# Optimization experiments

Measured on AMD Instinct MI355X. Metric: run time of the kernel, lower is better.

## Reference

```python
import jax, jax.numpy as jnp
import numpy as np


def setup_inputs() -> dict:
    key = jax.random.key(0)
    ks = jax.random.split(key, 6)
    B, U, E, D, P = 8, 1024, 1024, 256, 256
    return {
        "u_enc": jax.random.normal(ks[0], (B, U, D), dtype=jnp.float32),
        "e_enc": jax.random.normal(ks[1], (B, E, D), dtype=jnp.float32),
        "pair_enc": jax.random.normal(ks[2], (B, U, E), dtype=jnp.float32),
        "ue_mask": jax.random.uniform(ks[3], (B, U, E), dtype=jnp.float32),
        "w_kernel": jax.random.normal(ks[4], (D, P), dtype=jnp.float32) / np.sqrt(D).astype(np.float32),
        "w_bias": jnp.zeros((P,), dtype=jnp.float32),
        "bpp_w": jnp.ones((), dtype=jnp.float32),
        "bpp_b": jnp.zeros((), dtype=jnp.float32),
    }


def reference(u_enc, e_enc, pair_enc, ue_mask, w_kernel, w_bias, bpp_w, bpp_b):
    # OuterProductUpdate: shared Dense projection of u and e, then outer product.
    u_p = u_enc @ w_kernel + w_bias            # [B,U,P]
    e_p = e_enc @ w_kernel + w_bias            # [B,E,P]
    op = ue_mask * jnp.einsum('bup,bep->bue', u_p, e_p)  # [B,U,E]
    # Sigmoid gate over pair features.
    mask = ue_mask * jax.nn.sigmoid(bpp_w * pair_enc + bpp_b + op)  # [B,U,E]
    # Original: (mask[...,None] * concat(u_rep, e_rep)).sum(axis=(-2,-3)).
    # Algebraically identical without the UxEx2D intermediate:
    #   concat( sum_{u,e} mask * u_enc[u],  sum_{u,e} mask * e_enc[e] )
    u_part = jnp.einsum('bue,bud->bd', mask, u_enc)  # [B,D]
    e_part = jnp.einsum('bue,bed->bd', mask, e_enc)  # [B,D]
    return jnp.concatenate([u_part, e_part], axis=-1)  # [B,2D]
```

## Files before the change

### kernel.cpp

```cpp
#include <hip/hip_runtime.h>

#define BDIM 8
#define UDIM 1024
#define EDIM 1024
#define DDIM 256
#define PDIM 256

typedef __attribute__((ext_vector_type(8))) short bf16x8;
typedef __attribute__((ext_vector_type(4))) float f32x4;
typedef __attribute__((ext_vector_type(4))) unsigned short u16x4;

__device__ __forceinline__ short f2bf(float x) {
    unsigned u = __float_as_uint(x);
    unsigned r = (u + 0x7FFFu + ((u >> 16) & 1u)) >> 16;
    return (short)r;
}

__global__ __launch_bounds__(256) void prep_kernel(
    const float* __restrict__ w, ushort* __restrict__ wT,
    float* __restrict__ sums, float* __restrict__ out, int out_size)
{
    int n = blockIdx.x, k = threadIdx.x;
    wT[(size_t)n * PDIM + k] = (ushort)f2bf(w[(size_t)k * PDIM + n]);
    int g = n * 256 + k;
    if (g < BDIM * UDIM + BDIM * EDIM) sums[g] = 0.f;
    if (g < out_size) out[g] = 0.f;
}

__global__ __launch_bounds__(256) void proj_kernel(
    const float* __restrict__ u_enc, const float* __restrict__ e_enc,
    const ushort* __restrict__ wT, const float* __restrict__ bias,
    ushort* __restrict__ u_p, ushort* __restrict__ e_p)
{
    int row0 = blockIdx.x * 64;
    int col0 = blockIdx.y * 64;
    const float* A; ushort* C;
    if (row0 < BDIM * UDIM) { A = u_enc; C = u_p; }
    else                    { A = e_enc; C = e_p; row0 -= BDIM * UDIM; }

    int tid  = threadIdx.x;
    int wave = tid >> 6, lane = tid & 63;
    int m = lane & 15, quad = lane >> 4;

    const float*  aptr = A + (size_t)(row0 + wave * 16 + m) * DDIM + quad * 8;
    const ushort* bptr = wT + (size_t)(col0 + m * 4) * DDIM + quad * 8;

    float4 a[16];
    #pragma unroll
    for (int s = 0; s < 8; ++s) {
        a[2 * s]     = *(const float4*)(aptr + s * 32);
        a[2 * s + 1] = *(const float4*)(aptr + s * 32 + 4);
    }
    __builtin_amdgcn_sched_barrier(0);

    f32x4 acc[4] = {};

    #pragma unroll
    for (int s = 0; s < 8; ++s) {
        float4 a0 = a[2 * s], a1 = a[2 * s + 1];
        bf16x8 af;
        af[0] = f2bf(a0.x); af[1] = f2bf(a0.y); af[2] = f2bf(a0.z); af[3] = f2bf(a0.w);
        af[4] = f2bf(a1.x); af[5] = f2bf(a1.y); af[6] = f2bf(a1.z); af[7] = f2bf(a1.w);
        #pragma unroll
        for (int nt = 0; nt < 4; ++nt) {
            bf16x8 bfr = *(const bf16x8*)(bptr + (size_t)nt * DDIM + s * 32);
            acc[nt] = __builtin_amdgcn_mfma_f32_16x16x32_bf16(af, bfr, acc[nt], 0, 0, 0);
        }
    }

    float4 bv = *(const float4*)&bias[col0 + m * 4];
    #pragma unroll
    for (int r = 0; r < 4; ++r) {
        int row = row0 + wave * 16 + quad * 4 + r;
        u16x4 o;
        o[0] = (ushort)f2bf(acc[0][r] + bv.x);
        o[1] = (ushort)f2bf(acc[1][r] + bv.y);
        o[2] = (ushort)f2bf(acc[2][r] + bv.z);
        o[3] = (ushort)f2bf(acc[3][r] + bv.w);
        *(u16x4*)&C[(size_t)row * PDIM + col0 + m * 4] = o;
    }
}

__global__ __launch_bounds__(256) void fused_kernel(
    const ushort* __restrict__ u_p, const ushort* __restrict__ e_p,
    const float* __restrict__ pair_enc, const float* __restrict__ ue_mask,
    const float* __restrict__ bpp_w_p, const float* __restrict__ bpp_b_p,
    float* __restrict__ row_sums, float* __restrict__ col_sums)
{
    __shared__ float colred[4][64];

    int b  = blockIdx.y;
    int iu = blockIdx.x >> 4, ie = blockIdx.x & 15;
    int u0 = iu * 64, e0 = ie * 64;

    int tid  = threadIdx.x;
    int wave = tid >> 6, lane = tid & 63;
    int m = lane & 15, quad = lane >> 4;

    const float* pm = pair_enc + (size_t)b * UDIM * EDIM;
    const float* mm = ue_mask  + (size_t)b * UDIM * EDIM;

    float4 mv[4], pv[4];
    #pragma unroll
    for (int r = 0; r < 4; ++r) {
        size_t idx = (size_t)(u0 + wave * 16 + quad * 4 + r) * EDIM + e0 + m * 4;
        mv[r] = *(const float4*)&mm[idx];
        pv[r] = *(const float4*)&pm[idx];
    }
    __builtin_amdgcn_sched_barrier(0);

    const ushort* Au = u_p + (size_t)b * UDIM * PDIM + (size_t)(u0 + wave * 16 + m) * PDIM + quad * 8;
    const ushort* Be = e_p + (size_t)b * EDIM * PDIM + (size_t)(e0 + m * 4) * PDIM + quad * 8;

    f32x4 acc[4] = {};

    #pragma unroll
    for (int k0 = 0; k0 < PDIM; k0 += 32) {
        bf16x8 af = *(const bf16x8*)(Au + k0);
        #pragma unroll
        for (int nt = 0; nt < 4; ++nt) {
            bf16x8 bfr = *(const bf16x8*)(Be + (size_t)nt * PDIM + k0);
            acc[nt] = __builtin_amdgcn_mfma_f32_16x16x32_bf16(af, bfr, acc[nt], 0, 0, 0);
        }
    }

    float bw = bpp_w_p[0], bb = bpp_b_p[0];
    float rsum[4];
    float csum[4] = {0.f, 0.f, 0.f, 0.f};
    #pragma unroll
    for (int r = 0; r < 4; ++r) {
        float mvv[4] = {mv[r].x, mv[r].y, mv[r].z, mv[r].w};
        float pvv[4] = {pv[r].x, pv[r].y, pv[r].z, pv[r].w};
        float rs = 0.f;
        #pragma unroll
        for (int nt = 0; nt < 4; ++nt) {
            float arg = bw * pvv[nt] + bb + mvv[nt] * acc[nt][r];
            float s = mvv[nt] / (1.f + __expf(-arg));
            rs       += s;
            csum[nt] += s;
        }
        rsum[r] = rs;
    }

    #pragma unroll
    for (int r = 0; r < 4; ++r) {
        float v = rsum[r];
        v += __shfl_xor(v, 1); v += __shfl_xor(v, 2);
        v += __shfl_xor(v, 4); v += __shfl_xor(v, 8);
        if (m == 0)
            atomicAdd(&row_sums[(size_t)b * UDIM + u0 + wave * 16 + quad * 4 + r], v);
    }

    #pragma unroll
    for (int nt = 0; nt < 4; ++nt) {
        float v = csum[nt];
        v += __shfl_xor(v, 16); v += __shfl_xor(v, 32);
        if (quad == 0) colred[wave][m * 4 + nt] = v;
    }
    __syncthreads();

    if (tid < 64) {
        float v = colred[0][tid] + colred[1][tid] + colred[2][tid] + colred[3][tid];
        atomicAdd(&col_sums[(size_t)b * EDIM + e0 + tid], v);
    }
}

__global__ __launch_bounds__(256) void finish_kernel(
    const float* __restrict__ u_enc, const float* __restrict__ e_enc,
    const float* __restrict__ row_sums, const float* __restrict__ col_sums,
    float* __restrict__ out)
{
    int b = blockIdx.x;
    int half = blockIdx.y;
    int chunk = blockIdx.z;
    int d = threadIdx.x;

    const float* enc = half ? e_enc : u_enc;
    const float* s   = half ? col_sums : row_sums;

    int base = chunk * 16;
    float sv[16];
    #pragma unroll
    for (int u = 0; u < 16; ++u) sv[u] = s[(size_t)b * UDIM + base + u];

    float a0 = 0.f, a1 = 0.f, a2 = 0.f, a3 = 0.f;
    #pragma unroll
    for (int u = 0; u < 16; u += 4) {
        a0 += sv[u + 0] * enc[(size_t)(b * UDIM + base + u + 0) * DDIM + d];
        a1 += sv[u + 1] * enc[(size_t)(b * UDIM + base + u + 1) * DDIM + d];
        a2 += sv[u + 2] * enc[(size_t)(b * UDIM + base + u + 2) * DDIM + d];
        a3 += sv[u + 3] * enc[(size_t)(b * UDIM + base + u + 3) * DDIM + d];
    }
    atomicAdd(&out[(size_t)b * 2 * DDIM + half * DDIM + d], (a0 + a1) + (a2 + a3));
}

extern "C" void kernel_launch(void* const* d_in, const int* in_sizes, int n_in,
                              void* d_out, int out_size, void* d_ws, size_t ws_size,
                              hipStream_t stream)
{
    const float* u_enc    = (const float*)d_in[0];
    const float* e_enc    = (const float*)d_in[1];
    const float* pair_enc = (const float*)d_in[2];
    const float* ue_mask  = (const float*)d_in[3];
    const float* w_kernel = (const float*)d_in[4];
    const float* w_bias   = (const float*)d_in[5];
    const float* bpp_w    = (const float*)d_in[6];
    const float* bpp_b    = (const float*)d_in[7];
    float* out = (float*)d_out;

    ushort* u_p = (ushort*)d_ws;
    ushort* e_p = u_p + (size_t)BDIM * UDIM * PDIM;
    ushort* wT  = e_p + (size_t)BDIM * EDIM * PDIM;
    float* row_sums = (float*)(wT + (size_t)DDIM * PDIM);
    float* col_sums = row_sums + BDIM * UDIM;

    prep_kernel<<<dim3(256), 256, 0, stream>>>(w_kernel, wT, row_sums, out, out_size);

    proj_kernel<<<dim3(256, 4), 256, 0, stream>>>(u_enc, e_enc, wT, w_bias, u_p, e_p);

    fused_kernel<<<dim3(256, BDIM), 256, 0, stream>>>(u_p, e_p, pair_enc, ue_mask,
                                                      bpp_w, bpp_b, row_sums, col_sums);

    finish_kernel<<<dim3(BDIM, 2, 64), 256, 0, stream>>>(u_enc, e_enc, row_sums, col_sums, out);
}
```

Measured before the change: 182.0 us.

## Pipeline fused kernel with LDS double-buffered e_p tiles, persistent E-loop

```diff
diff --git a/kernel.cpp b/kernel.cpp
--- a/kernel.cpp
+++ b/kernel.cpp
@@ -10,10 +10,19 @@
 typedef __attribute__((ext_vector_type(4))) float f32x4;
 typedef __attribute__((ext_vector_type(4))) unsigned short u16x4;
 
+#define WAIT_VM8  0x0F78
+#define WAIT_VM0  0x0F70
+
 __device__ __forceinline__ short f2bf(float x) {
     unsigned u = __float_as_uint(x);
     unsigned r = (u + 0x7FFFu + ((u >> 16) & 1u)) >> 16;
     return (short)r;
+}
+
+__device__ __forceinline__ void dma16(const void* g, void* l) {
+    __builtin_amdgcn_global_load_lds((const __attribute__((address_space(1))) void*)g,
+                                     (__attribute__((address_space(3))) void*)l,
+                                     16, 0, 0);
 }
 
 __global__ __launch_bounds__(256) void prep_kernel(
@@ -33,7 +42,6 @@
     ushort* __restrict__ u_p, ushort* __restrict__ e_p)
 {
     int row0 = blockIdx.x * 64;
-    int col0 = blockIdx.y * 64;
     const float* A; ushort* C;
     if (row0 < BDIM * UDIM) { A = u_enc; C = u_p; }
     else                    { A = e_enc; C = e_p; row0 -= BDIM * UDIM; }
@@ -42,8 +50,7 @@
     int wave = tid >> 6, lane = tid & 63;
     int m = lane & 15, quad = lane >> 4;
 
-    const float*  aptr = A + (size_t)(row0 + wave * 16 + m) * DDIM + quad * 8;
-    const ushort* bptr = wT + (size_t)(col0 + m * 4) * DDIM + quad * 8;
+    const float* aptr = A + (size_t)(row0 + wave * 16 + m) * DDIM + quad * 8;
 
     float4 a[16];
     #pragma unroll
@@ -53,31 +60,37 @@
     }
     __builtin_amdgcn_sched_barrier(0);
 
-    f32x4 acc[4] = {};
-
+    bf16x8 af[8];
     #pragma unroll
     for (int s = 0; s < 8; ++s) {
         float4 a0 = a[2 * s], a1 = a[2 * s + 1];
-        bf16x8 af;
-        af[0] = f2bf(a0.x); af[1] = f2bf(a0.y); af[2] = f2bf(a0.z); af[3] = f2bf(a0.w);
-        af[4] = f2bf(a1.x); af[5] = f2bf(a1.y); af[6] = f2bf(a1.z); af[7] = f2bf(a1.w);
-        #pragma unroll
-        for (int nt = 0; nt < 4; ++nt) {
-            bf16x8 bfr = *(const bf16x8*)(bptr + (size_t)nt * DDIM + s * 32);
-            acc[nt] = __builtin_amdgcn_mfma_f32_16x16x32_bf16(af, bfr, acc[nt], 0, 0, 0);
-        }
-    }
-
-    float4 bv = *(const float4*)&bias[col0 + m * 4];
-    #pragma unroll
-    for (int r = 0; r < 4; ++r) {
-        int row = row0 + wave * 16 + quad * 4 + r;
-        u16x4 o;
-        o[0] = (ushort)f2bf(acc[0][r] + bv.x);
-        o[1] = (ushort)f2bf(acc[1][r] + bv.y);
-        o[2] = (ushort)f2bf(acc[2][r] + bv.z);
-        o[3] = (ushort)f2bf(acc[3][r] + bv.w);
-        *(u16x4*)&C[(size_t)row * PDIM + col0 + m * 4] = o;
+        af[s][0] = f2bf(a0.x); af[s][1] = f2bf(a0.y); af[s][2] = f2bf(a0.z); af[s][3] = f2bf(a0.w);
+        af[s][4] = f2bf(a1.x); af[s][5] = f2bf(a1.y); af[s][6] = f2bf(a1.z); af[s][7] = f2bf(a1.w);
+    }
+
+    #pragma unroll
+    for (int ct = 0; ct < 4; ++ct) {
+        const ushort* bptr = wT + (size_t)(ct * 64 + m * 4) * DDIM + quad * 8;
+        f32x4 acc[4] = {};
+        #pragma unroll
+        for (int ks = 0; ks < 8; ++ks) {
+            #pragma unroll
+            for (int nt = 0; nt < 4; ++nt) {
+                bf16x8 bfr = *(const bf16x8*)(bptr + (size_t)nt * DDIM + ks * 32);
+                acc[nt] = __builtin_amdgcn_mfma_f32_16x16x32_bf16(af[ks], bfr, acc[nt], 0, 0, 0);
+            }
+        }
+        float4 bv = *(const float4*)&bias[ct * 64 + m * 4];
+        #pragma unroll
+        for (int r = 0; r < 4; ++r) {
+            int row = row0 + wave * 16 + quad * 4 + r;
+            u16x4 o;
+            o[0] = (ushort)f2bf(acc[0][r] + bv.x);
+            o[1] = (ushort)f2bf(acc[1][r] + bv.y);
+            o[2] = (ushort)f2bf(acc[2][r] + bv.z);
+            o[3] = (ushort)f2bf(acc[3][r] + bv.w);
+            *(u16x4*)&C[(size_t)row * PDIM + ct * 64 + m * 4] = o;
+        }
     }
 }
 
@@ -87,81 +100,121 @@
     const float* __restrict__ bpp_w_p, const float* __restrict__ bpp_b_p,
     float* __restrict__ row_sums, float* __restrict__ col_sums)
 {
-    __shared__ float colred[4][64];
-
-    int b  = blockIdx.y;
-    int iu = blockIdx.x >> 4, ie = blockIdx.x & 15;
-    int u0 = iu * 64, e0 = ie * 64;
+    __shared__ __align__(16) ushort ep_lds[2][64 * 256];
+
+    int bx = blockIdx.x;
+    int b  = bx >> 5;
+    int iu = (bx >> 1) & 15;
+    int eh = bx & 1;
+    int u0 = iu * 64;
+    int ebase = eh * 512;
 
     int tid  = threadIdx.x;
     int wave = tid >> 6, lane = tid & 63;
     int m = lane & 15, quad = lane >> 4;
-
-    const float* pm = pair_enc + (size_t)b * UDIM * EDIM;
-    const float* mm = ue_mask  + (size_t)b * UDIM * EDIM;
-
-    float4 mv[4], pv[4];
+    int half = lane >> 5, slot = lane & 31;
+
+    const ushort* upb = u_p + (size_t)b * UDIM * PDIM;
+    const ushort* epb = e_p + (size_t)b * EDIM * PDIM;
+    const float*  pm  = pair_enc + (size_t)b * UDIM * EDIM;
+    const float*  mm  = ue_mask  + (size_t)b * UDIM * EDIM;
+
+    bf16x8 af[8];
+    {
+        const ushort* au = upb + (size_t)(u0 + wave * 16 + m) * PDIM + quad * 8;
+        #pragma unroll
+        for (int s = 0; s < 8; ++s) af[s] = *(const bf16x8*)(au + s * 32);
+    }
+
+    int prow = u0 + wave * 16 + quad * 4;
+    float4 pvr[2][4], mvr[2][4];
+
     #pragma unroll
     for (int r = 0; r < 4; ++r) {
-        size_t idx = (size_t)(u0 + wave * 16 + quad * 4 + r) * EDIM + e0 + m * 4;
-        mv[r] = *(const float4*)&mm[idx];
-        pv[r] = *(const float4*)&pm[idx];
-    }
-    __builtin_amdgcn_sched_barrier(0);
-
-    const ushort* Au = u_p + (size_t)b * UDIM * PDIM + (size_t)(u0 + wave * 16 + m) * PDIM + quad * 8;
-    const ushort* Be = e_p + (size_t)b * EDIM * PDIM + (size_t)(e0 + m * 4) * PDIM + quad * 8;
-
-    f32x4 acc[4] = {};
-
-    #pragma unroll
-    for (int k0 = 0; k0 < PDIM; k0 += 32) {
-        bf16x8 af = *(const bf16x8*)(Au + k0);
+        size_t idx = (size_t)(prow + r) * EDIM + ebase + m * 4;
+        mvr[0][r] = *(const float4*)&mm[idx];
+        pvr[0][r] = *(const float4*)&pm[idx];
+    }
+    #pragma unroll
+    for (int j = 0; j < 8; ++j) {
+        int lr = 16 * wave + 2 * j + half;
+        int kseg = slot ^ ((lr >> 2) & 7);
+        const ushort* g = epb + (size_t)(ebase + lr) * PDIM + kseg * 8;
+        dma16(g, &ep_lds[0][(16 * wave + 2 * j) * 256]);
+    }
+
+    float bw = bpp_w_p[0], bb = bpp_b_p[0];
+
+    #pragma unroll
+    for (int t = 0; t < 8; ++t) {
+        int cb = t & 1, nb = cb ^ 1;
+
+        if (t < 7) {
+            #pragma unroll
+            for (int r = 0; r < 4; ++r) {
+                size_t idx = (size_t)(prow + r) * EDIM + ebase + (t + 1) * 64 + m * 4;
+                mvr[nb][r] = *(const float4*)&mm[idx];
+                pvr[nb][r] = *(const float4*)&pm[idx];
+            }
+            #pragma unroll
+            for (int j = 0; j < 8; ++j) {
+                int lr = 16 * wave + 2 * j + half;
+                int kseg = slot ^ ((lr >> 2) & 7);
+                const ushort* g = epb + (size_t)(ebase + (t + 1) * 64 + lr) * PDIM + kseg * 8;
+                dma16(g, &ep_lds[nb][(16 * wave + 2 * j) * 256]);
+            }
+            __builtin_amdgcn_s_waitcnt(WAIT_VM8);
+        } else {
+            __builtin_amdgcn_s_waitcnt(WAIT_VM0);
+        }
+        __builtin_amdgcn_s_barrier();
+        __builtin_amdgcn_sched_barrier(0);
+
+        f32x4 acc[4] = {};
+        #pragma unroll
+        for (int ks = 0; ks < 8; ++ks) {
+            #pragma unroll
+            for (int nt = 0; nt < 4; ++nt) {
+                int row = m * 4 + nt;
+                int sl  = (ks * 4 + quad) ^ (m & 7);
+                bf16x8 bfr = *(const bf16x8*)&ep_lds[cb][row * 256 + sl * 8];
+                acc[nt] = __builtin_amdgcn_mfma_f32_16x16x32_bf16(af[ks], bfr, acc[nt], 0, 0, 0);
+            }
+        }
+        __builtin_amdgcn_s_barrier();
+
+        float rsum[4];
+        float csum[4] = {0.f, 0.f, 0.f, 0.f};
+        #pragma unroll
+        for (int r = 0; r < 4; ++r) {
+            float mvv[4] = {mvr[cb][r].x, mvr[cb][r].y, mvr[cb][r].z, mvr[cb][r].w};
+            float pvv[4] = {pvr[cb][r].x, pvr[cb][r].y, pvr[cb][r].z, pvr[cb][r].w};
+            float rs = 0.f;
+            #pragma unroll
+            for (int nt = 0; nt < 4; ++nt) {
+                float arg = bw * pvv[nt] + bb + mvv[nt] * acc[nt][r];
+                float s = mvv[nt] / (1.f + __expf(-arg));
+                rs       += s;
+                csum[nt] += s;
+            }
+            rsum[r] = rs;
+        }
+
+        #pragma unroll
+        for (int r = 0; r < 4; ++r) {
+            float v = rsum[r];
+            v += __shfl_xor(v, 1); v += __shfl_xor(v, 2);
+            v += __shfl_xor(v, 4); v += __shfl_xor(v, 8);
+            if (m == 0)
+                atomicAdd(&row_sums[(size_t)b * UDIM + prow + r], v);
+        }
         #pragma unroll
         for (int nt = 0; nt < 4; ++nt) {
-            bf16x8 bfr = *(const bf16x8*)(Be + (size_t)nt * PDIM + k0);
-            acc[nt] = __builtin_amdgcn_mfma_f32_16x16x32_bf16(af, bfr, acc[nt], 0, 0, 0);
-        }
-    }
-
-    float bw = bpp_w_p[0], bb = bpp_b_p[0];
-    float rsum[4];
-    float csum[4] = {0.f, 0.f, 0.f, 0.f};
-    #pragma unroll
-    for (int r = 0; r < 4; ++r) {
-        float mvv[4] = {mv[r].x, mv[r].y, mv[r].z, mv[r].w};
-        float pvv[4] = {pv[r].x, pv[r].y, pv[r].z, pv[r].w};
-        float rs = 0.f;
-        #pragma unroll
-        for (int nt = 0; nt < 4; ++nt) {
-            float arg = bw * pvv[nt] + bb + mvv[nt] * acc[nt][r];
-            float s = mvv[nt] / (1.f + __expf(-arg));
-            rs       += s;
-            csum[nt] += s;
-        }
-        rsum[r] = rs;
-    }
-
-    #pragma unroll
-    for (int r = 0; r < 4; ++r) {
-        float v = rsum[r];
-        v += __shfl_xor(v, 1); v += __shfl_xor(v, 2);
-        v += __shfl_xor(v, 4); v += __shfl_xor(v, 8);
-        if (m == 0)
-            atomicAdd(&row_sums[(size_t)b * UDIM + u0 + wave * 16 + quad * 4 + r], v);
-    }
-
-    #pragma unroll
-    for (int nt = 0; nt < 4; ++nt) {
-        float v = csum[nt];
-        v += __shfl_xor(v, 16); v += __shfl_xor(v, 32);
-        if (quad == 0) colred[wave][m * 4 + nt] = v;
-    }
-    __syncthreads();
-
-    if (tid < 64) {
-        float v = colred[0][tid] + colred[1][tid] + colred[2][tid] + colred[3][tid];
-        atomicAdd(&col_sums[(size_t)b * EDIM + e0 + tid], v);
+            float v = csum[nt];
+            v += __shfl_xor(v, 16); v += __shfl_xor(v, 32);
+            if (quad == 0)
+                atomicAdd(&col_sums[(size_t)b * EDIM + ebase + t * 64 + m * 4 + nt], v);
+        }
     }
 }
 
@@ -178,20 +231,22 @@
     const float* enc = half ? e_enc : u_enc;
     const float* s   = half ? col_sums : row_sums;
 
-    int base = chunk * 16;
-    float sv[16];
-    #pragma unroll
-    for (int u = 0; u < 16; ++u) sv[u] = s[(size_t)b * UDIM + base + u];
-
-    float a0 = 0.f, a1 = 0.f, a2 = 0.f, a3 = 0.f;
-    #pragma unroll
-    for (int u = 0; u < 16; u += 4) {
-        a0 += sv[u + 0] * enc[(size_t)(b * UDIM + base + u + 0) * DDIM + d];
-        a1 += sv[u + 1] * enc[(size_t)(b * UDIM + base + u + 1) * DDIM + d];
-        a2 += sv[u + 2] * enc[(size_t)(b * UDIM + base + u + 2) * DDIM + d];
-        a3 += sv[u + 3] * enc[(size_t)(b * UDIM + base + u + 3) * DDIM + d];
-    }
-    atomicAdd(&out[(size_t)b * 2 * DDIM + half * DDIM + d], (a0 + a1) + (a2 + a3));
+    int base = chunk * 32;
+    float sv[32];
+    #pragma unroll
+    for (int u = 0; u < 32; ++u) sv[u] = s[(size_t)b * UDIM + base + u];
+
+    float a[8] = {};
+    #pragma unroll
+    for (int u0 = 0; u0 < 4; ++u0) {
+        #pragma unroll
+        for (int j = 0; j < 8; ++j) {
+            int u = u0 * 8 + j;
+            a[j] += sv[u] * enc[(size_t)(b * UDIM + base + u) * DDIM + d];
+        }
+    }
+    float acc = ((a[0] + a[1]) + (a[2] + a[3])) + ((a[4] + a[5]) + (a[6] + a[7]));
+    atomicAdd(&out[(size_t)b * 2 * DDIM + half * DDIM + d], acc);
 }
 
 extern "C" void kernel_launch(void* const* d_in, const int* in_sizes, int n_in,
@@ -216,10 +271,10 @@
 
     prep_kernel<<<dim3(256), 256, 0, stream>>>(w_kernel, wT, row_sums, out, out_size);
 
-    proj_kernel<<<dim3(256, 4), 256, 0, stream>>>(u_enc, e_enc, wT, w_bias, u_p, e_p);
-
-    fused_kernel<<<dim3(256, BDIM), 256, 0, stream>>>(u_p, e_p, pair_enc, ue_mask,
-                                                      bpp_w, bpp_b, row_sums, col_sums);
-
-    finish_kernel<<<dim3(BDIM, 2, 64), 256, 0, stream>>>(u_enc, e_enc, row_sums, col_sums, out);
-}
+    proj_kernel<<<dim3(256), 256, 0, stream>>>(u_enc, e_enc, wT, w_bias, u_p, e_p);
+
+    fused_kernel<<<dim3(256), 256, 0, stream>>>(u_p, e_p, pair_enc, ue_mask,
+                                                bpp_w, bpp_b, row_sums, col_sums);
+
+    finish_kernel<<<dim3(BDIM, 2, 32), 256, 0, stream>>>(u_enc, e_enc, row_sums, col_sums, out);
+}
```

After: 200.7 us. +10.3%, slower.

## Split outer-product GEMM from sigmoid gating into separate streaming kernel

Applied to the files above, without the earlier changes.

```diff
diff --git a/kernel.cpp b/kernel.cpp
--- a/kernel.cpp
+++ b/kernel.cpp
@@ -15,6 +15,9 @@
     unsigned r = (u + 0x7FFFu + ((u >> 16) & 1u)) >> 16;
     return (short)r;
 }
+__device__ __forceinline__ float bf2f(unsigned short h) {
+    return __uint_as_float(((unsigned)h) << 16);
+}
 
 __global__ __launch_bounds__(256) void prep_kernel(
     const float* __restrict__ w, ushort* __restrict__ wT,
@@ -51,10 +54,8 @@
         a[2 * s]     = *(const float4*)(aptr + s * 32);
         a[2 * s + 1] = *(const float4*)(aptr + s * 32 + 4);
     }
-    __builtin_amdgcn_sched_barrier(0);
 
     f32x4 acc[4] = {};
-
     #pragma unroll
     for (int s = 0; s < 8; ++s) {
         float4 a0 = a[2 * s], a1 = a[2 * s + 1];
@@ -81,14 +82,10 @@
     }
 }
 
-__global__ __launch_bounds__(256) void fused_kernel(
+__global__ __launch_bounds__(256) void op_gemm_kernel(
     const ushort* __restrict__ u_p, const ushort* __restrict__ e_p,
-    const float* __restrict__ pair_enc, const float* __restrict__ ue_mask,
-    const float* __restrict__ bpp_w_p, const float* __restrict__ bpp_b_p,
-    float* __restrict__ row_sums, float* __restrict__ col_sums)
-{
-    __shared__ float colred[4][64];
-
+    ushort* __restrict__ op)
+{
     int b  = blockIdx.y;
     int iu = blockIdx.x >> 4, ie = blockIdx.x & 15;
     int u0 = iu * 64, e0 = ie * 64;
@@ -97,23 +94,10 @@
     int wave = tid >> 6, lane = tid & 63;
     int m = lane & 15, quad = lane >> 4;
 
-    const float* pm = pair_enc + (size_t)b * UDIM * EDIM;
-    const float* mm = ue_mask  + (size_t)b * UDIM * EDIM;
-
-    float4 mv[4], pv[4];
-    #pragma unroll
-    for (int r = 0; r < 4; ++r) {
-        size_t idx = (size_t)(u0 + wave * 16 + quad * 4 + r) * EDIM + e0 + m * 4;
-        mv[r] = *(const float4*)&mm[idx];
-        pv[r] = *(const float4*)&pm[idx];
-    }
-    __builtin_amdgcn_sched_barrier(0);
-
     const ushort* Au = u_p + (size_t)b * UDIM * PDIM + (size_t)(u0 + wave * 16 + m) * PDIM + quad * 8;
     const ushort* Be = e_p + (size_t)b * EDIM * PDIM + (size_t)(e0 + m * 4) * PDIM + quad * 8;
 
     f32x4 acc[4] = {};
-
     #pragma unroll
     for (int k0 = 0; k0 < PDIM; k0 += 32) {
         bf16x8 af = *(const bf16x8*)(Au + k0);
@@ -124,45 +108,81 @@
         }
     }
 
+    ushort* ob = op + (size_t)b * UDIM * EDIM;
+    #pragma unroll
+    for (int r = 0; r < 4; ++r) {
+        int row = u0 + wave * 16 + quad * 4 + r;
+        u16x4 o;
+        o[0] = (ushort)f2bf(acc[0][r]);
+        o[1] = (ushort)f2bf(acc[1][r]);
+        o[2] = (ushort)f2bf(acc[2][r]);
+        o[3] = (ushort)f2bf(acc[3][r]);
+        *(u16x4*)&ob[(size_t)row * EDIM + e0 + m * 4] = o;
+    }
+}
+
+__global__ __launch_bounds__(256) void stream_kernel(
+    const ushort* __restrict__ op, const float* __restrict__ pair_enc,
+    const float* __restrict__ ue_mask,
+    const float* __restrict__ bpp_w_p, const float* __restrict__ bpp_b_p,
+    float* __restrict__ row_sums, float* __restrict__ col_sums)
+{
+    int b = blockIdx.y;
+    int row0 = blockIdx.x * 16;
+    int t = threadIdx.x;
+    int lane = t & 63;
+    int e4 = t * 4;
+
+    const float*  pm = pair_enc + (size_t)b * UDIM * EDIM;
+    const float*  mm = ue_mask  + (size_t)b * UDIM * EDIM;
+    const ushort* ob = op       + (size_t)b * UDIM * EDIM;
     float bw = bpp_w_p[0], bb = bpp_b_p[0];
-    float rsum[4];
-    float csum[4] = {0.f, 0.f, 0.f, 0.f};
-    #pragma unroll
-    for (int r = 0; r < 4; ++r) {
-        float mvv[4] = {mv[r].x, mv[r].y, mv[r].z, mv[r].w};
-        float pvv[4] = {pv[r].x, pv[r].y, pv[r].z, pv[r].w};
-        float rs = 0.f;
-        #pragma unroll
-        for (int nt = 0; nt < 4; ++nt) {
-            float arg = bw * pvv[nt] + bb + mvv[nt] * acc[nt][r];
-            float s = mvv[nt] / (1.f + __expf(-arg));
-            rs       += s;
-            csum[nt] += s;
-        }
-        rsum[r] = rs;
-    }
-
-    #pragma unroll
-    for (int r = 0; r < 4; ++r) {
-        float v = rsum[r];
-        v += __shfl_xor(v, 1); v += __shfl_xor(v, 2);
-        v += __shfl_xor(v, 4); v += __shfl_xor(v, 8);
-        if (m == 0)
-            atomicAdd(&row_sums[(size_t)b * UDIM + u0 + wave * 16 + quad * 4 + r], v);
-    }
-
-    #pragma unroll
-    for (int nt = 0; nt < 4; ++nt) {
-        float v = csum[nt];
-        v += __shfl_xor(v, 16); v += __shfl_xor(v, 32);
-        if (quad == 0) colred[wave][m * 4 + nt] = v;
-    }
-    __syncthreads();
-
-    if (tid < 64) {
-        float v = colred[0][tid] + colred[1][tid] + colred[2][tid] + colred[3][tid];
-        atomicAdd(&col_sums[(size_t)b * EDIM + e0 + tid], v);
-    }
+
+    float cs0 = 0.f, cs1 = 0.f, cs2 = 0.f, cs3 = 0.f;
+
+    #pragma unroll 2
+    for (int r = 0; r < 16; r += 2) {
+        size_t i0 = (size_t)(row0 + r) * EDIM + e4;
+        size_t i1 = i0 + EDIM;
+        float4 p0 = *(const float4*)&pm[i0];
+        float4 k0 = *(const float4*)&mm[i0];
+        u16x4  o0 = *(const u16x4*)&ob[i0];
+        float4 p1 = *(const float4*)&pm[i1];
+        float4 k1 = *(const float4*)&mm[i1];
+        u16x4  o1 = *(const u16x4*)&ob[i1];
+
+        float pa[8] = {p0.x, p0.y, p0.z, p0.w, p1.x, p1.y, p1.z, p1.w};
+        float ka[8] = {k0.x, k0.y, k0.z, k0.w, k1.x, k1.y, k1.z, k1.w};
+        float oa[8] = {bf2f(o0[0]), bf2f(o0[1]), bf2f(o0[2]), bf2f(o0[3]),
+                       bf2f(o1[0]), bf2f(o1[1]), bf2f(o1[2]), bf2f(o1[3])};
+
+        float s[8];
+        #pragma unroll
+        for (int j = 0; j < 8; ++j) {
+            float arg = bw * pa[j] + bb + ka[j] * oa[j];
+            s[j] = ka[j] / (1.f + __expf(-arg));
+        }
+        cs0 += s[0] + s[4]; cs1 += s[1] + s[5];
+        cs2 += s[2] + s[6]; cs3 += s[3] + s[7];
+
+        float rs0 = (s[0] + s[1]) + (s[2] + s[3]);
+        float rs1 = (s[4] + s[5]) + (s[6] + s[7]);
+        rs0 += __shfl_xor(rs0, 1);  rs1 += __shfl_xor(rs1, 1);
+        rs0 += __shfl_xor(rs0, 2);  rs1 += __shfl_xor(rs1, 2);
+        rs0 += __shfl_xor(rs0, 4);  rs1 += __shfl_xor(rs1, 4);
+        rs0 += __shfl_xor(rs0, 8);  rs1 += __shfl_xor(rs1, 8);
+        rs0 += __shfl_xor(rs0, 16); rs1 += __shfl_xor(rs1, 16);
+        rs0 += __shfl_xor(rs0, 32); rs1 += __shfl_xor(rs1, 32);
+        if (lane == 0) {
+            atomicAdd(&row_sums[(size_t)b * UDIM + row0 + r],     rs0);
+            atomicAdd(&row_sums[(size_t)b * UDIM + row0 + r + 1], rs1);
+        }
+    }
+
+    atomicAdd(&col_sums[(size_t)b * EDIM + e4 + 0], cs0);
+    atomicAdd(&col_sums[(size_t)b * EDIM + e4 + 1], cs1);
+    atomicAdd(&col_sums[(size_t)b * EDIM + e4 + 2], cs2);
+    atomicAdd(&col_sums[(size_t)b * EDIM + e4 + 3], cs3);
 }
 
 __global__ __launch_bounds__(256) void finish_kernel(
@@ -178,20 +198,22 @@
     const float* enc = half ? e_enc : u_enc;
     const float* s   = half ? col_sums : row_sums;
 
-    int base = chunk * 16;
-    float sv[16];
-    #pragma unroll
-    for (int u = 0; u < 16; ++u) sv[u] = s[(size_t)b * UDIM + base + u];
-
-    float a0 = 0.f, a1 = 0.f, a2 = 0.f, a3 = 0.f;
-    #pragma unroll
-    for (int u = 0; u < 16; u += 4) {
-        a0 += sv[u + 0] * enc[(size_t)(b * UDIM + base + u + 0) * DDIM + d];
-        a1 += sv[u + 1] * enc[(size_t)(b * UDIM + base + u + 1) * DDIM + d];
-        a2 += sv[u + 2] * enc[(size_t)(b * UDIM + base + u + 2) * DDIM + d];
-        a3 += sv[u + 3] * enc[(size_t)(b * UDIM + base + u + 3) * DDIM + d];
-    }
-    atomicAdd(&out[(size_t)b * 2 * DDIM + half * DDIM + d], (a0 + a1) + (a2 + a3));
+    int base = chunk * 32;
+    float sv[32];
+    #pragma unroll
+    for (int u = 0; u < 32; ++u) sv[u] = s[(size_t)b * UDIM + base + u];
+
+    float a[8] = {};
+    #pragma unroll
+    for (int u0 = 0; u0 < 4; ++u0) {
+        #pragma unroll
+        for (int j = 0; j < 8; ++j) {
+            int u = u0 * 8 + j;
+            a[j] += sv[u] * enc[(size_t)(b * UDIM + base + u) * DDIM + d];
+        }
+    }
+    float acc = ((a[0] + a[1]) + (a[2] + a[3])) + ((a[4] + a[5]) + (a[6] + a[7]));
+    atomicAdd(&out[(size_t)b * 2 * DDIM + half * DDIM + d], acc);
 }
 
 extern "C" void kernel_launch(void* const* d_in, const int* in_sizes, int n_in,
@@ -210,7 +232,8 @@
 
     ushort* u_p = (ushort*)d_ws;
     ushort* e_p = u_p + (size_t)BDIM * UDIM * PDIM;
-    ushort* wT  = e_p + (size_t)BDIM * EDIM * PDIM;
+    ushort* op  = e_p + (size_t)BDIM * EDIM * PDIM;
+    ushort* wT  = op  + (size_t)BDIM * UDIM * EDIM;
     float* row_sums = (float*)(wT + (size_t)DDIM * PDIM);
     float* col_sums = row_sums + BDIM * UDIM;
 
@@ -218,8 +241,10 @@
 
     proj_kernel<<<dim3(256, 4), 256, 0, stream>>>(u_enc, e_enc, wT, w_bias, u_p, e_p);
 
-    fused_kernel<<<dim3(256, BDIM), 256, 0, stream>>>(u_p, e_p, pair_enc, ue_mask,
+    op_gemm_kernel<<<dim3(256, BDIM), 256, 0, stream>>>(u_p, e_p, op);
+
+    stream_kernel<<<dim3(64, BDIM), 256, 0, stream>>>(op, pair_enc, ue_mask,
                                                       bpp_w, bpp_b, row_sums, col_sums);
 
-    finish_kernel<<<dim3(BDIM, 2, 64), 256, 0, stream>>>(u_enc, e_enc, row_sums, col_sums, out);
-}
+    finish_kernel<<<dim3(BDIM, 2, 32), 256, 0, stream>>>(u_enc, e_enc, row_sums, col_sums, out);
+}
```

Measured after the change: 198.8 us. 9.2% more time.
